# Kernel optimization log

Measured on AMD Instinct MI355X. Metric: run time of the kernel, lower is better.

## Reference

```python
import jax, jax.numpy as jnp
import numpy as np
from jax.scipy.linalg import expm

CUTOFF = 8   # Fock cutoff D
M = 4        # qumodes
L = 2        # CVNeuralNet layers
N_OUT = 4
B = 4096     # batch
TWO_PI = 2.0 * np.pi

_n = jnp.arange(CUTOFF, dtype=jnp.float32)                      # number basis
_A = jnp.diag(jnp.sqrt(_n[1:]), 1).astype(jnp.complex64)        # annihilation op
_AD = _A.conj().T
_I = jnp.eye(CUTOFF, dtype=jnp.complex64)
_a1 = jnp.kron(_A, _I)   # mode-1 annihilation on 2-mode space
_a2 = jnp.kron(_I, _A)   # mode-2 annihilation on 2-mode space


def _disp(alpha):
    """Displacement gate D(alpha) = expm(alpha a^ - alpha* a) on truncated Fock space."""
    alpha = jnp.asarray(alpha, jnp.complex64)
    return expm(alpha * _AD - jnp.conj(alpha) * _A)


def _squeeze(r, phi):
    """Squeezing gate S(z) = expm((z* a^2 - z a^\u20202)/2), z = r e^{i phi}."""
    z = r * jnp.exp(1j * phi)
    return expm(0.5 * (jnp.conj(z) * (_A @ _A) - z * (_AD @ _AD)))


def _bs(theta, phi):
    """Beamsplitter BS(theta, phi) = expm(theta (e^{i phi} a1 a2^ - e^{-i phi} a1^ a2))."""
    H = theta * (jnp.exp(1j * phi) * _a1 @ _a2.conj().T - jnp.exp(-1j * phi) * _a1.conj().T @ _a2)
    return expm(H).reshape(CUTOFF, CUTOFF, CUTOFF, CUTOFF)


def _apply1(state, G, mode):
    # state: [B, D, D, D, D]; G: [D, D] acting on `mode`
    st = jnp.moveaxis(state, 1 + mode, -1)
    st = st @ G.T
    return jnp.moveaxis(st, -1, 1 + mode)


def _apply2(state, G, m1, m2):
    # G: [D, D, D, D] = (out1, out2, in1, in2)
    st = jnp.moveaxis(state, (1 + m1, 1 + m2), (-2, -1))
    st = jnp.einsum('ijkl,bxykl->bxyij', G, st.reshape(st.shape[0], -1, CUTOFF, CUTOFF, CUTOFF).reshape(st.shape)) if False else jnp.einsum('ijkl,b...kl->b...ij', G, st)
    return jnp.moveaxis(st, (-2, -1), (1 + m1, 1 + m2))


def _apply_diag(state, d, mode):
    shape = [1] * (M + 1)
    shape[1 + mode] = CUTOFF
    return state * d.reshape(shape)


def _interferometer(state, theta, phi, varphi):
    # PennyLane rectangular mesh: BS on (k, k+1) when (l + k) % 2 != 1, then rotations
    idx = 0
    for l in range(M):
        for k in range(M - 1):
            if (l + k) % 2 != 1:
                state = _apply2(state, _bs(theta[idx], phi[idx]), k, k + 1)
                idx += 1
    for m in range(M):
        state = _apply_diag(state, jnp.exp(1j * varphi[m] * _n), m)
    return state


def _forward(x, theta1, phi1, varphi1, r, phi_r, theta2, phi2, varphi2, a_amp, phi_a, kappa):
    # Displacement embedding: |psi0> = prod_m D(x_m)|0>, i.e. outer product of first columns
    Gs = jax.vmap(_disp)(x.reshape(-1)).reshape(x.shape[0], M, CUTOFF, CUTOFF)
    cols = Gs[..., 0]  # [B, M, D] : D(alpha)|0>
    state = jnp.einsum('bi,bj,bk,bl->bijkl', cols[:, 0], cols[:, 1], cols[:, 2], cols[:, 3])
    for l in range(L):
        state = _interferometer(state, theta1[l], phi1[l], varphi1[l])
        for m in range(M):
            state = _apply1(state, _squeeze(r[l, m], phi_r[l, m]), m)
        state = _interferometer(state, theta2[l], phi2[l], varphi2[l])
        for m in range(M):
            state = _apply1(state, _disp(a_amp[l, m] * jnp.exp(1j * phi_a[l, m])), m)
        for m in range(M):  # Kerr: diag exp(i kappa n^2)
            state = _apply_diag(state, jnp.exp(1j * kappa[l, m] * _n ** 2), m)
    # <X_i> = <a_i + a_i^> = 2 Re <psi| a_i |psi>  (hbar = 2 SF convention)
    outs = []
    for i in range(N_OUT):
        a_psi = _apply1(state, _A, i)
        exp_a = jnp.sum(jnp.conj(state) * a_psi, axis=tuple(range(1, M + 1)))
        outs.append(2.0 * jnp.real(exp_a))
    return jnp.stack(outs, axis=-1)  # [B, N_OUT]


def setup_inputs() -> dict:
    key = jax.random.key(0)
    ks = jax.random.split(key, 10)
    Kp = M * (M - 1) // 2
    u = lambda k, shape: jax.random.uniform(k, shape, jnp.float32, 0.0, TWO_PI)
    return {
        'x': jax.random.uniform(ks[0], (B, M), jnp.float32) * 0.5,
        'theta1': u(ks[1], (L, Kp)), 'phi1': u(ks[2], (L, Kp)), 'varphi1': u(ks[3], (L, M)),
        'r': jnp.full((L, M), 0.1, jnp.float32), 'phi_r': u(ks[4], (L, M)),
        'theta2': u(ks[5], (L, Kp)), 'phi2': u(ks[6], (L, Kp)), 'varphi2': u(ks[7], (L, M)),
        'a_amp': jnp.full((L, M), 0.1, jnp.float32), 'phi_a': u(ks[8], (L, M)),
        'kappa': u(ks[9], (L, M)),
    }


def reference(x, theta1, phi1, varphi1, r, phi_r, theta2, phi2, varphi2, a_amp, phi_a, kappa):
    return _forward(x, theta1, phi1, varphi1, r, phi_r, theta2, phi2, varphi2, a_amp, phi_a, kappa)
```

## Files before the change

kernel.cpp:

```cpp
#include <hip/hip_runtime.h>
#include <math.h>

#define WS_G1_OFF   (24*384)

typedef float v2f __attribute__((ext_vector_type(2)));
typedef float v4f __attribute__((ext_vector_type(4)));

__device__ __forceinline__ void cmac_s(v2f& acc, v2f s, v2f g){
  asm("v_pk_fma_f32 %0, %1, %2, %0 op_sel_hi:[0,1,1]\n\t"
      "v_pk_fma_f32 %0, %1, %2, %0 op_sel:[1,1,0] op_sel_hi:[1,0,1] neg_lo:[1,0,0]"
      : "+v"(acc) : "v"(s), "s"(g));
}
__device__ __forceinline__ v2f cmul_s0(v2f s, v2f g){
  v2f acc;
  asm("v_pk_fma_f32 %0, %1, %2, 0 op_sel_hi:[0,1,1]\n\t"
      "v_pk_fma_f32 %0, %1, %2, %0 op_sel:[1,1,0] op_sel_hi:[1,0,1] neg_lo:[1,0,0]"
      : "=&v"(acc) : "v"(s), "s"(g));
  return acc;
}
__device__ __forceinline__ void cmac_v(v2f& acc, v2f s, v2f g){
  asm("v_pk_fma_f32 %0, %1, %2, %0 op_sel_hi:[0,1,1]\n\t"
      "v_pk_fma_f32 %0, %1, %2, %0 op_sel:[1,1,0] op_sel_hi:[1,0,1] neg_lo:[1,0,0]"
      : "+v"(acc) : "v"(s), "v"(g));
}

__global__ __launch_bounds__(256) void setup_bs(
    const float* __restrict__ th1, const float* __restrict__ ph1,
    const float* __restrict__ th2, const float* __restrict__ ph2,
    float2* __restrict__ ws)
{
  __shared__ float2 bufA[4096];
  __shared__ float2 bufB[4096];
  const int g = blockIdx.x;
  const int t = threadIdx.x;
  const int l = g/12, intf = (g%12)/6, pos = g%6;
  const float th = (intf ? th2 : th1)[l*6+pos];
  const float ph = (intf ? ph2 : ph1)[l*6+pos];
  float nrm = fabsf(th)*14.0f;
  int sq = 0;
  if (nrm > 2.0f) sq = (int)ceilf(log2f(nrm*0.5f));
  const float tc  = th * ldexpf(1.0f, -sq);
  const float cph = cosf(ph), sph = sinf(ph);

  float2* cur = bufA; float2* nxt = bufB;
  for (int e=0;e<16;e++){ int idx=e*256+t;
    cur[idx] = make_float2(((idx>>6)==(idx&63))?1.f:0.f, 0.f); }
  __syncthreads();
  for (int k=12;k>=1;k--){
    const float inv = 1.0f/(float)k;
    for (int e=0;e<16;e++){
      const int idx=e*256+t; const int row=idx>>6, c=idx&63;
      const int m1=row>>3, m2=row&7;
      float vx=0.f, vy=0.f;
      if (m1<7 && m2>=1){
        const float mag = tc*sqrtf((float)((m1+1)*m2));
        const float2 q = cur[((m1+1)*8+(m2-1))*64 + c];
        vx += mag*(cph*q.x - sph*q.y);
        vy += mag*(cph*q.y + sph*q.x);
      }
      if (m1>=1 && m2<7){
        const float mag = tc*sqrtf((float)(m1*(m2+1)));
        const float2 q = cur[((m1-1)*8+(m2+1))*64 + c];
        vx -= mag*(cph*q.x + sph*q.y);
        vy -= mag*(cph*q.y - sph*q.x);
      }
      vx *= inv; vy *= inv;
      if (row==c) vx += 1.0f;
      nxt[idx] = make_float2(vx,vy);
    }
    __syncthreads();
    float2* tmp=cur; cur=nxt; nxt=tmp;
  }
  for (int si=0; si<sq; si++){
    for (int e=0;e<16;e++){
      const int idx=e*256+t; const int row=idx>>6, c=idx&63;
      const float2* Arow = cur + row*64;
      v2f acc = (v2f){0.f,0.f};
      for (int q=0;q<64;q+=2){
        const v4f ap = *(const v4f*)&Arow[q];
        const v2f b0 = *(const v2f*)&cur[q*64+c];
        const v2f b1 = *(const v2f*)&cur[(q+1)*64+c];
        cmac_v(acc, b0, (v2f){ap.x,ap.y});
        cmac_v(acc, b1, (v2f){ap.z,ap.w});
      }
      nxt[idx] = make_float2(acc.x, acc.y);
    }
    __syncthreads();
    float2* tmp=cur; cur=nxt; nxt=tmp;
  }
  for (int e=t; e<384; e+=256){
    int rem = e, N = 0, S_=0, SR_=0;
    for (; N<15; N++){
      S_  = 8 - ((N<7)?(7-N):(N-7));
      SR_ = (S_+1)&~1;
      if (rem < S_*SR_) break;
      rem -= S_*SR_;
    }
    float2 v = make_float2(0.f,0.f);
    if (N < 15){
      const int o = rem / SR_, ti = rem % SR_;
      if (ti < S_){
        const int T0 = (N>7)?(N-7):0;
        const int j = 7*(T0+o)+N, k = 7*(T0+ti)+N;
        v = cur[j*64 + k];
      }
    }
    ws[g*384 + e] = v;
  }
}

__global__ __launch_bounds__(128) void setup_small(
    const float* __restrict__ rr,  const float* __restrict__ phr,
    const float* __restrict__ aa,  const float* __restrict__ pha,
    const float* __restrict__ vph1,const float* __restrict__ vph2,
    const float* __restrict__ kap,
    float2* __restrict__ ws_g1)
{
  const int g = blockIdx.x, t = threadIdx.x;
  __shared__ float2 h8[64], bufA[64], bufB[64];
  const int isSq = (g < 8);
  const int gi = isSq ? g : (g-8);
  const int li = gi>>2, m = gi&3;
  const float p1 = isSq ? rr[li*4+m]  : aa[li*4+m];
  const float p2 = isSq ? phr[li*4+m] : pha[li*4+m];
  const float nrm = fabsf(p1)*6.0f;
  int sq = 0; if (nrm > 2.0f) sq = (int)ceilf(log2f(nrm*0.5f));
  const float sc = ldexpf(1.0f,-sq);
  const float cp = cosf(p2), sp = sinf(p2);
  if (t < 64){
    const int row=t>>3, c=t&7;
    float2 v = make_float2(0.f,0.f);
    if (isSq){
      if (c == row+2){ const float mg = 0.5f*p1*sqrtf((float)((row+1)*(row+2)));
                       v = make_float2( mg*cp, -mg*sp); }
      else if (c+2 == row){ const float mg = 0.5f*p1*sqrtf((float)((row-1)*row));
                       v = make_float2(-mg*cp, -mg*sp); }
    } else {
      if (c+1 == row){ const float mg = p1*sqrtf((float)row);
                       v = make_float2( mg*cp,  mg*sp); }
      else if (c == row+1){ const float mg = p1*sqrtf((float)(row+1));
                       v = make_float2(-mg*cp,  mg*sp); }
    }
    h8[t]   = make_float2(v.x*sc, v.y*sc);
    bufA[t] = make_float2((row==c)?1.f:0.f, 0.f);
  }
  __syncthreads();
  float2* cur=bufA; float2* nxt=bufB;
  for (int k=12;k>=1;k--){
    const float inv = 1.0f/(float)k;
    if (t<64){
      const int row=t>>3, c=t&7;
      float vx=0.f, vy=0.f;
      for (int q=0;q<8;q++){
        const float2 a_=h8[row*8+q], b_=cur[q*8+c];
        vx += a_.x*b_.x - a_.y*b_.y; vy += a_.x*b_.y + a_.y*b_.x;
      }
      vx*=inv; vy*=inv; if (row==c) vx += 1.f;
      nxt[t]=make_float2(vx,vy);
    }
    __syncthreads();
    float2* tmp=cur; cur=nxt; nxt=tmp;
  }
  for (int si=0; si<sq; si++){
    if (t<64){
      const int row=t>>3, c=t&7;
      float vx=0.f, vy=0.f;
      for (int q=0;q<8;q++){
        const float2 a_=cur[row*8+q], b_=cur[q*8+c];
        vx += a_.x*b_.x - a_.y*b_.y; vy += a_.x*b_.y + a_.y*b_.x;
      }
      nxt[t]=make_float2(vx,vy);
    }
    __syncthreads();
    float2* tmp=cur; cur=nxt; nxt=tmp;
  }
  if (t<64){
    const int kk=t>>3, j=t&7;
    const float2 v = cur[j*8+kk];
    float ang;
    if (isSq) ang = vph1[li*4+m]*(float)kk;
    else      ang = vph2[li*4+m]*(float)kk + kap[li*4+m]*(float)(j*j);
    const float ca = cosf(ang), sa = sinf(ang);
    ws_g1[g*64 + t] = make_float2(v.x*ca - v.y*sa, v.x*sa + v.y*ca);
  }
}


template<int PM>
__device__ __forceinline__ constexpr int koff(int k){
  return (PM==0) ? 65*k : ((PM==1) ? (8*k + (k>>3)) : k);
}

template<int NN,int PM>
__device__ __forceinline__ void bs_sector(const float2* __restrict__ gsec,
                                          float2* __restrict__ Sm, int sb)
{
  constexpr int S_ = 8 - ((NN<7)?(7-NN):(NN-7));
  constexpr int T0 = (NN>7)?(NN-7):0;
  constexpr int SR = (S_+1)&~1;
  v2f sv[S_];
#pragma unroll
  for (int i=0;i<S_;i++)
    sv[i] = *(const v2f*)&Sm[sb + koff<PM>(7*(T0+i)+NN)];
#pragma unroll
  for (int o=0;o<S_;o++){
    v2f acc = cmul_s0(sv[0], *(const v2f*)&gsec[o*SR]);
#pragma unroll
    for (int i=1;i<S_;i++)
      cmac_s(acc, sv[i], *(const v2f*)&gsec[o*SR+i]);
    *(v2f*)&Sm[sb + koff<PM>(7*(T0+o)+NN)] = acc;
  }
}

template<int PM>
__device__ __forceinline__ void bs_gate(const float2* __restrict__ gb,
                                        float2* __restrict__ Sm, int sb, int wvu)
{
  if (wvu==0){
    bs_sector<7 ,PM>(gb+156, Sm, sb);
  } else if (wvu==1){
    bs_sector<6 ,PM>(gb+100, Sm, sb);
    bs_sector<14,PM>(gb+374, Sm, sb);
  } else if (wvu==2){
    bs_sector<8 ,PM>(gb+220, Sm, sb);
    bs_sector<0 ,PM>(gb+0,   Sm, sb);
  } else if (wvu==3){
    bs_sector<5 ,PM>(gb+64,  Sm, sb);
    bs_sector<13,PM>(gb+370, Sm, sb);
  } else if (wvu==4){
    bs_sector<9 ,PM>(gb+276, Sm, sb);
    bs_sector<1 ,PM>(gb+2,   Sm, sb);
  } else if (wvu==5){
    bs_sector<4 ,PM>(gb+34,  Sm, sb);
    bs_sector<12,PM>(gb+358, Sm, sb);
  } else if (wvu==6){
    bs_sector<10,PM>(gb+312, Sm, sb);
    bs_sector<2 ,PM>(gb+6,   Sm, sb);
  } else {
    bs_sector<3 ,PM>(gb+18,  Sm, sb);
    bs_sector<11,PM>(gb+342, Sm, sb);
  }
  __syncthreads();
}

template<int M>
__device__ __forceinline__ void one_mode(const float2* __restrict__ gb,
                                         float2* __restrict__ Sm, int t)
{
  constexpr int ek = (M==0)?520:((M==1)?65:((M==2)?8:1));
  const int v = t;
  int base;
  if constexpr (M==0)      base = 65*(v>>6) + 8*((v>>3)&7) + (v&7);
  else if constexpr (M==1) base = 520*(v>>6) + 8*((v>>3)&7) + (v&7);
  else if constexpr (M==2) base = 520*(((v>>3)&1)|(((v>>7)&3)<<1)) + 65*((v>>4)&7) + (v&7);
  else                     base = 520*((v>>4)&7) + 65*(v&7) + 8*(((v>>3)&1)|(((v>>7)&3)<<1));
  v2f acc[8];
#pragma unroll
  for (int k=0;k<8;k++){
    const v2f sA = *(const v2f*)&Sm[base + ek*k];
#pragma unroll
    for (int j=0;j<8;j++){
      const v2f g = *(const v2f*)&gb[k*8+j];
      if (k==0) acc[j] = cmul_s0(sA, g);
      else      cmac_s(acc[j], sA, g);
    }
  }
#pragma unroll
  for (int j=0;j<8;j++) *(v2f*)&Sm[base + ek*j] = acc[j];
  __syncthreads();
}

__global__ __launch_bounds__(512,2) void qnn_main(
    const float* __restrict__ x, const float2* __restrict__ ws,
    float* __restrict__ out)
{
  __shared__ __align__(16) float2 S[4160];
  __shared__ float colf[32];
  __shared__ float red[32];
  const int b = blockIdx.x, t = threadIdx.x;
  const int lane = t & 63;
  const int wvu = __builtin_amdgcn_readfirstlane(t>>6);
  const int i2c = (t>>3)&7, i3c = t&7;

  if (t < 32){
    const int m = t>>3, n = t&7;
    const float xv = x[b*4+m];
    float val = expf(-0.5f*xv*xv);
    for (int q=1;q<=n;q++) val *= xv * rsqrtf((float)q);
    colf[t] = val;
  }
  __syncthreads();
  {
    const float c23 = colf[16+i2c]*colf[24+i3c];
    const float c1  = colf[8+wvu];
#pragma unroll
    for (int e=0;e<8;e++){
      const int idx = e*512 + t;
      S[idx + (idx>>6)] = make_float2(colf[e] * c1 * c23, 0.f);
    }
  }
  __syncthreads();

  const int sbP0 = lane;
  const int sbP1 = 520*(lane>>3) + (lane&7);
  const int sbP2 = 520*(lane>>3) + 65*(lane&7);
  const float2* ws_g1 = ws + WS_G1_OFF;

#pragma unroll 1
  for (int seg=0; seg<4; seg++){
    const float2* bsg = ws + seg*(6*384);
#pragma unroll 1
    for (int q=0; q<6; q++){
      const float2* gq = bsg + q*384;
      const int pm = (q>=3)? (q-3) : q;
      if (pm==0)      bs_gate<0>(gq, S, sbP0, wvu);
      else if (pm==1) bs_gate<2>(gq, S, sbP2, wvu);
      else            bs_gate<1>(gq, S, sbP1, wvu);
    }
    const int l = seg>>1, r = seg&1;
    const float2* om = ws_g1 + (r*8 + l*4)*64;
    one_mode<0>(om,     S, t);
    one_mode<1>(om+64,  S, t);
    one_mode<2>(om+128, S, t);
    one_mode<3>(om+192, S, t);
  }

  const float w1 = sqrtf((float)(wvu+1));
  const float w2 = sqrtf((float)(i2c+1)), w3 = sqrtf((float)(i3c+1));
  float am0=0.f, am1=0.f, am2=0.f, am3=0.f;
#pragma unroll
  for (int e=0;e<8;e++){
    const int idx = e*512 + t;
    const float2 a = S[idx + (idx>>6)];
    if (e < 7){
      const int j2 = idx + 512; const float2 bz = S[j2 + (j2>>6)];
      am0 = fmaf(a.x*bz.x + a.y*bz.y, sqrtf((float)(e+1)), am0);
    }
    if (wvu < 7){
      const int j2 = idx + 64; const float2 bz = S[j2 + (j2>>6)];
      am1 = fmaf(a.x*bz.x + a.y*bz.y, w1, am1);
    }
    if (i2c < 7){
      const int j2 = idx + 8; const float2 bz = S[j2 + (j2>>6)];
      am2 = fmaf(a.x*bz.x + a.y*bz.y, w2, am2);
    }
    if (i3c < 7){
      const int j2 = idx + 1; const float2 bz = S[j2 + (j2>>6)];
      am3 = fmaf(a.x*bz.x + a.y*bz.y, w3, am3);
    }
  }
#pragma unroll
  for (int o=32;o;o>>=1){
    am0 += __shfl_down(am0,o,64);
    am1 += __shfl_down(am1,o,64);
    am2 += __shfl_down(am2,o,64);
    am3 += __shfl_down(am3,o,64);
  }
  __syncthreads();
  if ((t&63)==0){
    red[wvu*4+0]=am0; red[wvu*4+1]=am1; red[wvu*4+2]=am2; red[wvu*4+3]=am3;
  }
  __syncthreads();
  if (t<4){
    float s = 0.f;
#pragma unroll
    for (int w=0;w<8;w++) s += red[w*4+t];
    out[b*4+t] = 2.f*s;
  }
}

extern "C" void kernel_launch(void* const* d_in, const int* in_sizes, int n_in,
                              void* d_out, int out_size, void* d_ws, size_t ws_size,
                              hipStream_t stream)
{
  const float* x    = (const float*)d_in[0];
  const float* th1  = (const float*)d_in[1];
  const float* ph1  = (const float*)d_in[2];
  const float* vph1 = (const float*)d_in[3];
  const float* rr   = (const float*)d_in[4];
  const float* phr  = (const float*)d_in[5];
  const float* th2  = (const float*)d_in[6];
  const float* ph2  = (const float*)d_in[7];
  const float* vph2 = (const float*)d_in[8];
  const float* aa   = (const float*)d_in[9];
  const float* pha  = (const float*)d_in[10];
  const float* kap  = (const float*)d_in[11];
  float2* ws  = (float2*)d_ws;
  float*  out = (float*)d_out;
  const int B = in_sizes[0] / 4;

  hipLaunchKernelGGL(setup_bs, dim3(24), dim3(256), 0, stream, th1, ph1, th2, ph2, ws);
  hipLaunchKernelGGL(setup_small, dim3(16), dim3(128), 0, stream,
                     rr, phr, aa, pha, vph1, vph2, kap, ws + WS_G1_OFF);
  hipLaunchKernelGGL(qnn_main, dim3(B), dim3(512), 0, stream, x, ws, out);
}
```

Baseline: 485.8 us.

## Rebalance beamsplitter sector work across waves by splitting output rows

The beamsplitter gate work is redistributed across the eight waves. Large sectors now have their output rows split between two waves, so each wave does a similar number of complex MACs instead of wave 0 alone handling the largest sector. Because several waves now read the same sector inputs before anyone writes, all input taps are loaded into registers first and a new barrier separates the read phase from the compute/write phase. This adds an extra __syncthreads per gate and more register pressure (up to 15 taps per lane).

Result: slower. 533.7 us (+9.9%).

```diff
diff --git a/kernel.cpp b/kernel.cpp
--- a/kernel.cpp
+++ b/kernel.cpp
@@ -192,22 +192,30 @@
 }
 
 template<int NN,int PM>
-__device__ __forceinline__ void bs_sector(const float2* __restrict__ gsec,
-                                          float2* __restrict__ Sm, int sb)
+__device__ __forceinline__ void bs_read(const float2* __restrict__ Sm, int sb,
+                                        v2f* tap)
+{
+  constexpr int S_ = 8 - ((NN<7)?(7-NN):(NN-7));
+  constexpr int T0 = (NN>7)?(NN-7):0;
+#pragma unroll
+  for (int i=0;i<S_;i++)
+    tap[i] = *(const v2f*)&Sm[sb + koff<PM>(7*(T0+i)+NN)];
+}
+
+template<int NN,int PM,int O0,int O1>
+__device__ __forceinline__ void bs_comp(const float2* __restrict__ gsec,
+                                        float2* __restrict__ Sm, int sb,
+                                        const v2f* tap)
 {
   constexpr int S_ = 8 - ((NN<7)?(7-NN):(NN-7));
   constexpr int T0 = (NN>7)?(NN-7):0;
   constexpr int SR = (S_+1)&~1;
-  v2f sv[S_];
-#pragma unroll
-  for (int i=0;i<S_;i++)
-    sv[i] = *(const v2f*)&Sm[sb + koff<PM>(7*(T0+i)+NN)];
-#pragma unroll
-  for (int o=0;o<S_;o++){
-    v2f acc = cmul_s0(sv[0], *(const v2f*)&gsec[o*SR]);
+#pragma unroll
+  for (int o=O0;o<O1;o++){
+    v2f acc = cmul_s0(tap[0], *(const v2f*)&gsec[o*SR]);
 #pragma unroll
     for (int i=1;i<S_;i++)
-      cmac_s(acc, sv[i], *(const v2f*)&gsec[o*SR+i]);
+      cmac_s(acc, tap[i], *(const v2f*)&gsec[o*SR+i]);
     *(v2f*)&Sm[sb + koff<PM>(7*(T0+o)+NN)] = acc;
   }
 }
@@ -216,30 +224,37 @@
 __device__ __forceinline__ void bs_gate(const float2* __restrict__ gb,
                                         float2* __restrict__ Sm, int sb, int wvu)
 {
-  if (wvu==0){
-    bs_sector<7 ,PM>(gb+156, Sm, sb);
-  } else if (wvu==1){
-    bs_sector<6 ,PM>(gb+100, Sm, sb);
-    bs_sector<14,PM>(gb+374, Sm, sb);
-  } else if (wvu==2){
-    bs_sector<8 ,PM>(gb+220, Sm, sb);
-    bs_sector<0 ,PM>(gb+0,   Sm, sb);
-  } else if (wvu==3){
-    bs_sector<5 ,PM>(gb+64,  Sm, sb);
-    bs_sector<13,PM>(gb+370, Sm, sb);
-  } else if (wvu==4){
-    bs_sector<9 ,PM>(gb+276, Sm, sb);
-    bs_sector<1 ,PM>(gb+2,   Sm, sb);
-  } else if (wvu==5){
-    bs_sector<4 ,PM>(gb+34,  Sm, sb);
-    bs_sector<12,PM>(gb+358, Sm, sb);
-  } else if (wvu==6){
-    bs_sector<10,PM>(gb+312, Sm, sb);
-    bs_sector<2 ,PM>(gb+6,   Sm, sb);
-  } else {
-    bs_sector<3 ,PM>(gb+18,  Sm, sb);
-    bs_sector<11,PM>(gb+342, Sm, sb);
-  }
+  v2f tap[15];
+  if (wvu==0){      bs_read<7 ,PM>(Sm,sb,tap);   bs_read<1 ,PM>(Sm,sb,tap+8); }
+  else if (wvu==1){ bs_read<7 ,PM>(Sm,sb,tap);   bs_read<4 ,PM>(Sm,sb,tap+8); }
+  else if (wvu==2){ bs_read<6 ,PM>(Sm,sb,tap);   bs_read<0 ,PM>(Sm,sb,tap+7); }
+  else if (wvu==3){ bs_read<6 ,PM>(Sm,sb,tap);   bs_read<5 ,PM>(Sm,sb,tap+7); }
+  else if (wvu==4){ bs_read<8 ,PM>(Sm,sb,tap);   bs_read<14,PM>(Sm,sb,tap+7); }
+  else if (wvu==5){ bs_read<8 ,PM>(Sm,sb,tap);   bs_read<9 ,PM>(Sm,sb,tap+7); }
+  else if (wvu==6){ bs_read<4 ,PM>(Sm,sb,tap);   bs_read<10,PM>(Sm,sb,tap+5);
+                    bs_read<2 ,PM>(Sm,sb,tap+10); bs_read<13,PM>(Sm,sb,tap+13); }
+  else {            bs_read<3 ,PM>(Sm,sb,tap);   bs_read<11,PM>(Sm,sb,tap+4);
+                    bs_read<12,PM>(Sm,sb,tap+8); }
+  __syncthreads();
+  if (wvu==0){      bs_comp<7 ,PM,0,5>(gb+156,Sm,sb,tap);
+                    bs_comp<1 ,PM,0,2>(gb+2,  Sm,sb,tap+8); }
+  else if (wvu==1){ bs_comp<7 ,PM,5,8>(gb+156,Sm,sb,tap);
+                    bs_comp<4 ,PM,0,4>(gb+34, Sm,sb,tap+8); }
+  else if (wvu==2){ bs_comp<6 ,PM,0,6>(gb+100,Sm,sb,tap);
+                    bs_comp<0 ,PM,0,1>(gb+0,  Sm,sb,tap+7); }
+  else if (wvu==3){ bs_comp<6 ,PM,6,7>(gb+100,Sm,sb,tap);
+                    bs_comp<5 ,PM,0,6>(gb+64, Sm,sb,tap+7); }
+  else if (wvu==4){ bs_comp<8 ,PM,0,6>(gb+220,Sm,sb,tap);
+                    bs_comp<14,PM,0,1>(gb+374,Sm,sb,tap+7); }
+  else if (wvu==5){ bs_comp<8 ,PM,6,7>(gb+220,Sm,sb,tap);
+                    bs_comp<9 ,PM,0,6>(gb+276,Sm,sb,tap+7); }
+  else if (wvu==6){ bs_comp<4 ,PM,4,5>(gb+34, Sm,sb,tap);
+                    bs_comp<10,PM,0,5>(gb+312,Sm,sb,tap+5);
+                    bs_comp<2 ,PM,0,3>(gb+6,  Sm,sb,tap+10);
+                    bs_comp<13,PM,0,2>(gb+370,Sm,sb,tap+13); }
+  else {            bs_comp<3 ,PM,0,4>(gb+18, Sm,sb,tap);
+                    bs_comp<11,PM,0,4>(gb+342,Sm,sb,tap+4);
+                    bs_comp<12,PM,0,3>(gb+358,Sm,sb,tap+8); }
   __syncthreads();
 }
 
```
